# Performance work log

Measured on AMD Instinct MI355X. Metric: run time of the kernel, lower is better.

The kernel has to match this reference:

```python
import jax, jax.numpy as jnp
import numpy as np

NUM_GROUPS = 32
EPS = 1e-6

def group_norm(x, gamma, beta):
    # x: [B, C, P]
    B, C, P = x.shape
    xg = x.reshape(B, NUM_GROUPS, C // NUM_GROUPS, P)
    mean = jnp.mean(xg, axis=(2, 3), keepdims=True)
    var = jnp.var(xg, axis=(2, 3), keepdims=True)
    xn = ((xg - mean) * jax.lax.rsqrt(var + EPS)).reshape(B, C, P)
    return xn * gamma[None, :, None] + beta[None, :, None]

def conv1x1(h, w, b):
    # h: [B, C, P], w: [C_out, C_in], b: [C_out]
    return jnp.einsum('oc,bcp->bop', w, h) + b[None, :, None]

def setup_inputs() -> dict:
    key = jax.random.key(0)
    ks = jax.random.split(key, 10)
    B, C, P = 4, 512, 4096
    x = jax.random.normal(ks[0], (B, C, P), dtype=jnp.float32)
    gn_gamma = jnp.ones((C,), dtype=jnp.float32)
    gn_beta = jnp.zeros((C,), dtype=jnp.float32)
    s = 0.02
    wq = jax.random.normal(ks[1], (C, C), dtype=jnp.float32) * s
    bq = jax.random.normal(ks[2], (C,), dtype=jnp.float32) * s
    wk = jax.random.normal(ks[3], (C, C), dtype=jnp.float32) * s
    bk = jax.random.normal(ks[4], (C,), dtype=jnp.float32) * s
    wv = jax.random.normal(ks[5], (C, C), dtype=jnp.float32) * s
    bv = jax.random.normal(ks[6], (C,), dtype=jnp.float32) * s
    wo = jax.random.normal(ks[7], (C, C), dtype=jnp.float32) * s
    bo = jax.random.normal(ks[8], (C,), dtype=jnp.float32) * s
    return {"x": x, "gn_gamma": gn_gamma, "gn_beta": gn_beta,
            "wq": wq, "bq": bq, "wk": wk, "bk": bk,
            "wv": wv, "bv": bv, "wo": wo, "bo": bo}

def reference(x, gn_gamma, gn_beta, wq, bq, wk, bk, wv, bv, wo, bo):
    h = group_norm(x, gn_gamma, gn_beta)          # [B, C, P]
    q = conv1x1(h, wq, bq)                         # [B, C, P]
    k = conv1x1(h, wk, bk)                         # [B, C, P]
    v = conv1x1(h, wv, bv)                         # [B, C, P]
    C = q.shape[1]
    scale = 1.0 / jnp.sqrt(jnp.float32(C))
    # w[b, i, j] = sum_c q[b, c, i] * k[b, c, j]
    w = jnp.einsum('bci,bcj->bij', q, k) * scale   # [B, P, P]
    w = jax.nn.softmax(w, axis=2)
    # h_out[b, c, i] = sum_j v[b, c, j] * w[b, i, j]
    h = jnp.einsum('bij,bcj->bci', w, v)           # [B, C, P]
    h = conv1x1(h, wo, bo)
    return x + h
```

## Files before the change

### kernel.cpp

```cpp
#include <hip/hip_runtime.h>
#include <stdint.h>


typedef __bf16 bf16_t;
typedef __attribute__((ext_vector_type(4))) __bf16 bf16x4;
typedef __attribute__((ext_vector_type(8))) __bf16 bf16x8;
typedef __attribute__((ext_vector_type(4))) float floatx4;
typedef __attribute__((ext_vector_type(8))) int intx8;

constexpr int CDIM = 512;
constexpr int PDIM = 4096;

__device__ __forceinline__ void ld_g2l(const void* g, void* l) {
  __builtin_amdgcn_global_load_lds(
      (const __attribute__((address_space(1))) void*)g,
      (__attribute__((address_space(3))) void*)l,
      16, 0, 0);
}

__device__ __forceinline__ uint32_t pk_fp8x4(float a, float b, float c,
                                             float d) {
  int r = __builtin_amdgcn_cvt_pk_fp8_f32(a, b, 0, false);
  r = __builtin_amdgcn_cvt_pk_fp8_f32(c, d, r, true);
  return (uint32_t)r;
}

__device__ __forceinline__ int sigma_row(int r) {
  return (r & 64) + ((r & 15) << 2) + ((r >> 4) & 3);
}

enum { EPI_QK = 0, EPI_V = 1, EPI_OUT = 4, EPI_EXP = 2, EPI_PV = 5 };

template <int EPI, int TM>
__global__ __launch_bounds__(256) void gemm_tn(
    const bf16_t* __restrict__ A, const bf16_t* __restrict__ B, int K,
    int lda, int ldb, long sAb, long sBb, long sCb, void* __restrict__ Cv,
    int ldc, const float* __restrict__ bias, const float* __restrict__ xres) {
  constexpr int MI = TM / 32;
  constexpr int WROWS = TM / 2;
  __shared__ bf16_t Asm[TM * 64];
  __shared__ bf16_t Bsm[128 * 64];

  const int tid = threadIdx.x;
  const int w = tid >> 6, l = tid & 63;
  const int m0 = blockIdx.y * TM, n0 = blockIdx.x * 128;
  const int bz = blockIdx.z;

  const bf16_t* Ab = A + (long)bz * sAb + (long)m0 * lda;
  const bf16_t* Bb = B + (long)bz * sBb + (long)n0 * ldb;

  const int r0 = 8 * w + (l >> 3);
  const int schunk = (l & 7) ^ (l >> 3);
  const bf16_t* ga = Ab + (long)r0 * lda + schunk * 8;
  bf16_t* lA = Asm + (8 * w) * 64;
  bf16_t* lB = Bsm + (8 * w) * 64;

  const int wr = w >> 1, wc = w & 1;
  const int fr = l & 15, fq = l >> 4, l7 = l & 7;

  floatx4 acc[MI][4];
  floatx4 zz = {0.f, 0.f, 0.f, 0.f};
#pragma unroll
  for (int i = 0; i < MI; i++)
#pragma unroll
    for (int j = 0; j < 4; j++) acc[i][j] = zz;

  for (int kb = 0; kb < K; kb += 64) {
#pragma unroll
    for (int p = 0; p < 4; p++) {
      if (p < TM / 32) ld_g2l(ga + (long)p * 32 * lda + kb, lA + p * 2048);
      const int sig = sigma_row(r0 + 32 * p);
      ld_g2l(Bb + (long)sig * ldb + schunk * 8 + kb, lB + p * 2048);
    }
    __syncthreads();
#pragma unroll
    for (int ks = 0; ks < 2; ks++) {
      bf16x8 af[MI], bfv[4];
      const int ch = (ks * 4 + fq);
#pragma unroll
      for (int mi = 0; mi < MI; mi++) {
        int row = wr * WROWS + mi * 16 + fr;
        af[mi] = *(const bf16x8*)(Asm + row * 64 + ((ch ^ l7) * 8));
      }
#pragma unroll
      for (int ni = 0; ni < 4; ni++) {
        int row = wc * 64 + ni * 16 + fr;
        bfv[ni] = *(const bf16x8*)(Bsm + row * 64 + ((ch ^ l7) * 8));
      }
#pragma unroll
      for (int mi = 0; mi < MI; mi++)
#pragma unroll
        for (int ni = 0; ni < 4; ni++)
          acc[mi][ni] = __builtin_amdgcn_mfma_f32_16x16x32_bf16(
              af[mi], bfv[ni], acc[mi][ni], 0, 0, 0);
    }
    __syncthreads();
  }

  const int rb = fq * 4;
  const int gcolb = n0 + wc * 64 + 4 * fr;
#pragma unroll
  for (int mi = 0; mi < MI; mi++) {
#pragma unroll
    for (int i = 0; i < 4; i++) {
      const int grow = m0 + wr * WROWS + mi * 16 + rb + i;
      float v0 = acc[mi][0][i], v1 = acc[mi][1][i];
      float v2 = acc[mi][2][i], v3 = acc[mi][3][i];
      if constexpr (EPI == EPI_QK) {
        const float4 b4 = *(const float4*)(bias + gcolb);
        *(uint32_t*)((uint8_t*)Cv + (long)bz * sCb + (long)grow * ldc +
                     gcolb) =
            pk_fp8x4(v0 + b4.x, v1 + b4.y, v2 + b4.z, v3 + b4.w);
      } else if constexpr (EPI == EPI_V) {
        const float bb = bias[grow];
        uint32_t d = pk_fp8x4(v0 + bb, v1 + bb, v2 + bb, v3 + bb);
        *(uint32_t*)((uint8_t*)Cv + (long)bz * sCb + (long)grow * ldc +
                     gcolb) = d;
      } else {
        int ob = gcolb >> 12, op = gcolb & 4095;
        long o = ((long)ob * CDIM + grow) * PDIM + op;
        const float4 xr = *(const float4*)(xres + o);
        const float bb = bias[grow];
        float4 ov = {v0 + bb + xr.x, v1 + bb + xr.y, v2 + bb + xr.z,
                     v3 + bb + xr.w};
        *(float4*)((float*)Cv + o) = ov;
      }
    }
  }
}

template <int EPI, int TM, int SA>
__global__ __launch_bounds__(256) void gemm_f8(
    const uint8_t* __restrict__ A, const uint8_t* __restrict__ B, int K,
    int lda, int ldb, long sAb, long sBb, long sCb, void* __restrict__ Cv,
    int ldc, float* __restrict__ rsum) {
  constexpr int MI = TM / 32;
  constexpr int WROWS = TM / 2;
  __shared__ uint8_t Asm[TM * 128];
  __shared__ uint8_t Bsm[128 * 128];

  const int tid = threadIdx.x;
  const int w = tid >> 6, l = tid & 63;
  const int m0 = blockIdx.y * TM, n0 = blockIdx.x * 128;
  const int bz = blockIdx.z;

  const uint8_t* Ab = A + (long)bz * sAb + (long)m0 * lda;
  const uint8_t* Bb = B + (long)bz * sBb + (long)n0 * ldb;

  const int r0 = 8 * w + (l >> 3);
  const int schunk = (l & 7) ^ (l >> 3);
  const uint8_t* ga = Ab + (long)r0 * lda + schunk * 16;
  uint8_t* lA = Asm + (8 * w) * 128;
  uint8_t* lB = Bsm + (8 * w) * 128;

  const int wr = w >> 1, wc = w & 1;
  const int fr = l & 15, fq = l >> 4, l7 = l & 7;

  floatx4 acc[MI][4];
#pragma unroll
  for (int i = 0; i < MI; i++)
#pragma unroll
    for (int j = 0; j < 4; j++) acc[i][j] = floatx4{0.f, 0.f, 0.f, 0.f};

  const int s0 = ((2 * fq) ^ l7) * 16;
  const int s1 = ((2 * fq + 1) ^ l7) * 16;

  for (int kb = 0; kb < K; kb += 128) {
#pragma unroll
    for (int p = 0; p < 4; p++) {
      if (p < MI) ld_g2l(ga + (long)p * 32 * lda + kb, lA + p * 4096);
      const int sig = sigma_row(r0 + 32 * p);
      ld_g2l(Bb + (long)sig * ldb + schunk * 16 + kb, lB + p * 4096);
    }
    __syncthreads();

    intx8 af[MI];
#pragma unroll
    for (int mi = 0; mi < MI; mi++) {
      const uint8_t* base = Asm + (wr * WROWS + mi * 16 + fr) * 128;
      uint4 x0 = *(const uint4*)(base + s0);
      uint4 x1 = *(const uint4*)(base + s1);
      af[mi] = intx8{(int)x0.x, (int)x0.y, (int)x0.z, (int)x0.w,
                     (int)x1.x, (int)x1.y, (int)x1.z, (int)x1.w};
    }
#pragma unroll
    for (int ni = 0; ni < 4; ni++) {
      const uint8_t* base = Bsm + (wc * 64 + ni * 16 + fr) * 128;
      uint4 y0 = *(const uint4*)(base + s0);
      uint4 y1 = *(const uint4*)(base + s1);
      intx8 bf = intx8{(int)y0.x, (int)y0.y, (int)y0.z, (int)y0.w,
                       (int)y1.x, (int)y1.y, (int)y1.z, (int)y1.w};
#pragma unroll
      for (int mi = 0; mi < MI; mi++)
        acc[mi][ni] = __builtin_amdgcn_mfma_scale_f32_16x16x128_f8f6f4(
            af[mi], bf, acc[mi][ni], 0, 0, 0, SA, 0, 127);
    }
    __syncthreads();
  }

  const int rb = fq * 4;
  const int gcolb = n0 + wc * 64 + 4 * fr;
#pragma unroll
  for (int mi = 0; mi < MI; mi++) {
#pragma unroll
    for (int i = 0; i < 4; i++) {
      const int grow = m0 + wr * WROWS + mi * 16 + rb + i;
      if constexpr (EPI == EPI_EXP) {
        float p0 = exp2f(acc[mi][0][i]), p1 = exp2f(acc[mi][1][i]);
        float p2 = exp2f(acc[mi][2][i]), p3 = exp2f(acc[mi][3][i]);
        *(uint32_t*)((uint8_t*)Cv + (long)bz * sCb + (long)grow * ldc +
                     gcolb) = pk_fp8x4(p0, p1, p2, p3);
        float rowacc = (p0 + p1) + (p2 + p3);
        rowacc += __shfl_xor(rowacc, 1);
        rowacc += __shfl_xor(rowacc, 2);
        rowacc += __shfl_xor(rowacc, 4);
        rowacc += __shfl_xor(rowacc, 8);
        if (fr == 0) atomicAdd(&rsum[(long)bz * PDIM + grow], rowacc);
      } else {
        const float inv =
            __builtin_amdgcn_rcpf(rsum[(long)bz * PDIM + grow]);
        bf16x4 o = {(bf16_t)(acc[mi][0][i] * inv),
                    (bf16_t)(acc[mi][1][i] * inv),
                    (bf16_t)(acc[mi][2][i] * inv),
                    (bf16_t)(acc[mi][3][i] * inv)};
        *(bf16x4*)((bf16_t*)Cv + (long)bz * sCb + (long)grow * ldc + gcolb) =
            o;
      }
    }
  }
}

__global__ __launch_bounds__(256) void gn_stats(const float* __restrict__ x,
                                                float2* __restrict__ part) {
  const int i = blockIdx.x;
  const float4* xp = (const float4*)(x + (long)i * 8192);
  float s0 = 0.f, s1 = 0.f;
  for (int j = threadIdx.x; j < 2048; j += 256) {
    float4 v = xp[j];
    s0 += v.x + v.y + v.z + v.w;
    s1 += v.x * v.x + v.y * v.y + v.z * v.z + v.w * v.w;
  }
  for (int o = 32; o; o >>= 1) {
    s0 += __shfl_xor(s0, o);
    s1 += __shfl_xor(s1, o);
  }
  __shared__ float r0[4], r1[4];
  if ((threadIdx.x & 63) == 0) {
    r0[threadIdx.x >> 6] = s0;
    r1[threadIdx.x >> 6] = s1;
  }
  __syncthreads();
  if (threadIdx.x == 0)
    part[i] = make_float2(r0[0] + r0[1] + r0[2] + r0[3],
                          r1[0] + r1[1] + r1[2] + r1[3]);
}

__global__ __launch_bounds__(256) void gn_norm(
    const float* __restrict__ x, const float* __restrict__ gamma,
    const float* __restrict__ beta, const float2* __restrict__ part,
    bf16_t* __restrict__ h_t) {
  const int b = blockIdx.x >> 7;
  const int p0 = (blockIdx.x & 127) * 32;
  const int t = threadIdx.x;
  __shared__ float gmS[512], btS[512];
  __shared__ float gmean[32], grstd[32];
  __shared__ __align__(16) bf16_t tile[32 * 520];

  if (t < 32) {
    const float2* pp = part + (b * 32 + t) * 8;
    float s0 = 0.f, s1 = 0.f;
#pragma unroll
    for (int s = 0; s < 8; s++) {
      float2 v = pp[s];
      s0 += v.x;
      s1 += v.y;
    }
    float mean = s0 * (1.f / 65536.f);
    float var = s1 * (1.f / 65536.f) - mean * mean;
    gmean[t] = mean;
    grstd[t] = rsqrtf(var + 1e-6f);
  }
  __syncthreads();
  for (int c = t; c < 512; c += 256) {
    float g = gamma[c] * grstd[c >> 4];
    gmS[c] = g;
    btS[c] = beta[c] - gmean[c >> 4] * g;
  }
  __syncthreads();

  const int cc = t >> 3, pcol = (t & 7) * 4;
  for (int pass = 0; pass < 16; pass++) {
    int c = pass * 32 + cc;
    float4 v = *(const float4*)(x + ((long)(b * 512 + c)) * 4096 + p0 + pcol);
    float g = gmS[c], bb = btS[c];
    tile[(pcol + 0) * 520 + c] = (bf16_t)(v.x * g + bb);
    tile[(pcol + 1) * 520 + c] = (bf16_t)(v.y * g + bb);
    tile[(pcol + 2) * 520 + c] = (bf16_t)(v.z * g + bb);
    tile[(pcol + 3) * 520 + c] = (bf16_t)(v.w * g + bb);
  }
  __syncthreads();
  const int p = t >> 3;
  bf16_t* orow = h_t + ((long)(b * 4096 + p0 + p)) * 512;
  const bf16_t* trow = tile + p * 520;
#pragma unroll
  for (int j = 0; j < 8; j++) {
    int ch = (t & 7) + 8 * j;
    *(uint4*)(orow + ch * 8) = *(const uint4*)(trow + ch * 8);
  }
}

__global__ __launch_bounds__(256) void cvt_weights(
    const float* __restrict__ wq, const float* __restrict__ wk,
    const float* __restrict__ wv, const float* __restrict__ wo,
    const float* __restrict__ bq, const float* __restrict__ bk,
    bf16_t* __restrict__ out, float* __restrict__ bqk) {
  constexpr float QW = 1.02013936f;
  int i = blockIdx.x * 256 + threadIdx.x;
  out[i] = (bf16_t)(wq[i] * QW);
  out[262144 + i] = (bf16_t)wk[i];
  out[2 * 262144 + i] = (bf16_t)wv[i];
  out[3 * 262144 + i] = (bf16_t)wo[i];
  if (i < 512)
    bqk[i] = bq[i] * QW;
  else if (i < 1024)
    bqk[i] = bk[i - 512];
}

extern "C" void kernel_launch(void* const* d_in, const int* in_sizes, int n_in,
                              void* d_out, int out_size, void* d_ws,
                              size_t ws_size, hipStream_t stream) {
  const float* x = (const float*)d_in[0];
  const float* gamma = (const float*)d_in[1];
  const float* beta = (const float*)d_in[2];
  const float* wq = (const float*)d_in[3];
  const float* bq = (const float*)d_in[4];
  const float* wk = (const float*)d_in[5];
  const float* bk = (const float*)d_in[6];
  const float* wv = (const float*)d_in[7];
  const float* bv = (const float*)d_in[8];
  const float* wo = (const float*)d_in[9];
  const float* bo = (const float*)d_in[10];

  char* ws = (char*)d_ws;
  bf16_t* h_t = (bf16_t*)(ws);
  uint8_t* qk8 = (uint8_t*)(ws + (16l << 20));
  uint8_t* v_c = (uint8_t*)(ws + (48l << 20));
  bf16_t* h_at = (bf16_t*)(ws + (64l << 20));
  bf16_t* w_b = (bf16_t*)(ws + (80l << 20));
  float2* part = (float2*)(ws + (83l << 20));
  float* bqk = (float*)(ws + (83l << 20) + (64l << 10));
  float* rsum = (float*)(ws + (83l << 20) + (128l << 10));
  uint8_t* Sbuf = (uint8_t*)(ws + (84l << 20));

  const long sQK8 = (long)PDIM * 1024;
  const long sS = (long)PDIM * PDIM;

  hipMemsetAsync(rsum, 0, 4 * PDIM * sizeof(float), stream);
  cvt_weights<<<1024, 256, 0, stream>>>(wq, wk, wv, wo, bq, bk, w_b, bqk);
  gn_stats<<<1024, 256, 0, stream>>>(x, part);
  gn_norm<<<512, 256, 0, stream>>>(x, gamma, beta, part, h_t);
  gemm_tn<EPI_QK, 128><<<dim3(8, 128, 1), 256, 0, stream>>>(
      h_t, w_b, 512, 512, 512, 0, 0, 0, qk8, 1024, bqk, nullptr);
  gemm_tn<EPI_V, 64><<<dim3(128, 8, 1), 256, 0, stream>>>(
      w_b + 2 * 262144, h_t, 512, 512, 512, 0, 0, 0, v_c, 16384, bv, nullptr);
  gemm_f8<EPI_EXP, 128, 123><<<dim3(32, 32, 4), 256, 0, stream>>>(
      qk8, qk8 + 512, 512, 1024, 1024, sQK8, sQK8, sS, Sbuf, 4096, rsum);
  gemm_f8<EPI_PV, 64, 127><<<dim3(4, 64, 4), 256, 0, stream>>>(
      Sbuf, v_c, 4096, 4096, 16384, sS, 4096, (long)PDIM * CDIM, h_at, 512,
      rsum);
  gemm_tn<EPI_OUT, 64><<<dim3(128, 8, 1), 256, 0, stream>>>(
      w_b + 3 * 262144, h_at, 512, 512, 512, 0, 0, 0, d_out, 4096, bo, x);
}
```

Before: 295.4 us.

## Enlarge GEMM tiles, add XCD-aware block remap, replace rowsum atomics with partials

The GEMM kernels are generalised to a configurable thread count, and the QK projection and QK^T exp kernels move to 256-row tiles with 512 threads. The PV kernel moves to 128-row tiles. Block indices are remapped so neighbouring tiles land on the same XCD and share L2. The atomicAdd row-sum accumulation is replaced by per-column-block partial writes plus a separate reduce kernel, which also removes the memset. The goals are less operand reloading, better L2 locality, and no atomic contention, at the cost of higher register and LDS pressure per block and one extra launch.

```diff
diff --git a/kernel.cpp b/kernel.cpp
--- a/kernel.cpp
+++ b/kernel.cpp
@@ -29,22 +29,39 @@
   return (r & 64) + ((r & 15) << 2) + ((r >> 4) & 3);
 }
 
+__device__ __forceinline__ void xcd_remap(int& bx, int& by, int& bz) {
+  const int gx = gridDim.x, gy = gridDim.y;
+  const int nwg = gx * gy * (int)gridDim.z;
+  int lin = bx + gx * (by + gy * bz);
+  int wg = (lin & 7) * (nwg >> 3) + (lin >> 3);
+  bx = wg % gx;
+  int t = wg / gx;
+  by = t % gy;
+  bz = t / gy;
+}
+
 enum { EPI_QK = 0, EPI_V = 1, EPI_OUT = 4, EPI_EXP = 2, EPI_PV = 5 };
 
-template <int EPI, int TM>
-__global__ __launch_bounds__(256) void gemm_tn(
+template <int EPI, int TM, int NT, bool SWZ>
+__global__ __launch_bounds__(NT) void gemm_tn(
     const bf16_t* __restrict__ A, const bf16_t* __restrict__ B, int K,
     int lda, int ldb, long sAb, long sBb, long sCb, void* __restrict__ Cv,
     int ldc, const float* __restrict__ bias, const float* __restrict__ xres) {
-  constexpr int MI = TM / 32;
-  constexpr int WROWS = TM / 2;
+  constexpr int NW = NT / 64;
+  constexpr int WROWS = TM / (NW / 2);
+  constexpr int MI = WROWS / 16;
+  constexpr int RB = NT / 8;
+  constexpr int AB = TM / RB;
+  constexpr int BB = 128 / RB;
+  constexpr int PMAX = AB > BB ? AB : BB;
   __shared__ bf16_t Asm[TM * 64];
   __shared__ bf16_t Bsm[128 * 64];
 
   const int tid = threadIdx.x;
   const int w = tid >> 6, l = tid & 63;
-  const int m0 = blockIdx.y * TM, n0 = blockIdx.x * 128;
-  const int bz = blockIdx.z;
+  int bx = blockIdx.x, by = blockIdx.y, bz = blockIdx.z;
+  if constexpr (SWZ) xcd_remap(bx, by, bz);
+  const int m0 = by * TM, n0 = bx * 128;
 
   const bf16_t* Ab = A + (long)bz * sAb + (long)m0 * lda;
   const bf16_t* Bb = B + (long)bz * sBb + (long)n0 * ldb;
@@ -67,10 +84,12 @@
 
   for (int kb = 0; kb < K; kb += 64) {
 #pragma unroll
-    for (int p = 0; p < 4; p++) {
-      if (p < TM / 32) ld_g2l(ga + (long)p * 32 * lda + kb, lA + p * 2048);
-      const int sig = sigma_row(r0 + 32 * p);
-      ld_g2l(Bb + (long)sig * ldb + schunk * 8 + kb, lB + p * 2048);
+    for (int p = 0; p < PMAX; p++) {
+      if (p < AB) ld_g2l(ga + (long)(p * RB) * lda + kb, lA + p * RB * 64);
+      if (p < BB) {
+        const int sig = sigma_row(r0 + RB * p);
+        ld_g2l(Bb + (long)sig * ldb + schunk * 8 + kb, lB + p * RB * 64);
+      }
     }
     __syncthreads();
 #pragma unroll
@@ -129,20 +148,26 @@
   }
 }
 
-template <int EPI, int TM, int SA>
-__global__ __launch_bounds__(256) void gemm_f8(
+template <int EPI, int TM, int SA, int NT>
+__global__ __launch_bounds__(NT) void gemm_f8(
     const uint8_t* __restrict__ A, const uint8_t* __restrict__ B, int K,
     int lda, int ldb, long sAb, long sBb, long sCb, void* __restrict__ Cv,
     int ldc, float* __restrict__ rsum) {
-  constexpr int MI = TM / 32;
-  constexpr int WROWS = TM / 2;
+  constexpr int NW = NT / 64;
+  constexpr int WROWS = TM / (NW / 2);
+  constexpr int MI = WROWS / 16;
+  constexpr int RB = NT / 8;
+  constexpr int AB = TM / RB;
+  constexpr int BB = 128 / RB;
+  constexpr int PMAX = AB > BB ? AB : BB;
   __shared__ uint8_t Asm[TM * 128];
   __shared__ uint8_t Bsm[128 * 128];
 
   const int tid = threadIdx.x;
   const int w = tid >> 6, l = tid & 63;
-  const int m0 = blockIdx.y * TM, n0 = blockIdx.x * 128;
-  const int bz = blockIdx.z;
+  int bx = blockIdx.x, by = blockIdx.y, bz = blockIdx.z;
+  xcd_remap(bx, by, bz);
+  const int m0 = by * TM, n0 = bx * 128;
 
   const uint8_t* Ab = A + (long)bz * sAb + (long)m0 * lda;
   const uint8_t* Bb = B + (long)bz * sBb + (long)n0 * ldb;
@@ -167,10 +192,12 @@
 
   for (int kb = 0; kb < K; kb += 128) {
 #pragma unroll
-    for (int p = 0; p < 4; p++) {
-      if (p < MI) ld_g2l(ga + (long)p * 32 * lda + kb, lA + p * 4096);
-      const int sig = sigma_row(r0 + 32 * p);
-      ld_g2l(Bb + (long)sig * ldb + schunk * 16 + kb, lB + p * 4096);
+    for (int p = 0; p < PMAX; p++) {
+      if (p < AB) ld_g2l(ga + (long)(p * RB) * lda + kb, lA + p * RB * 128);
+      if (p < BB) {
+        const int sig = sigma_row(r0 + RB * p);
+        ld_g2l(Bb + (long)sig * ldb + schunk * 16 + kb, lB + p * RB * 128);
+      }
     }
     __syncthreads();
 
@@ -215,7 +242,8 @@
         rowacc += __shfl_xor(rowacc, 2);
         rowacc += __shfl_xor(rowacc, 4);
         rowacc += __shfl_xor(rowacc, 8);
-        if (fr == 0) atomicAdd(&rsum[(long)bz * PDIM + grow], rowacc);
+        if (fr == 0)
+          rsum[((long)(bz * 64 + bx * 2 + wc)) * PDIM + grow] = rowacc;
       } else {
         const float inv =
             __builtin_amdgcn_rcpf(rsum[(long)bz * PDIM + grow]);
@@ -228,6 +256,17 @@
       }
     }
   }
+}
+
+__global__ __launch_bounds__(256) void rsum_reduce(
+    const float* __restrict__ part2, float* __restrict__ rsum) {
+  const int r = blockIdx.x * 256 + threadIdx.x;
+  const int bz = r >> 12, row = r & 4095;
+  const float* p = part2 + ((long)bz * 64) * PDIM + row;
+  float s = 0.f;
+#pragma unroll
+  for (int j = 0; j < 64; j++) s += p[(long)j * PDIM];
+  rsum[r] = s;
 }
 
 __global__ __launch_bounds__(256) void gn_stats(const float* __restrict__ x,
@@ -343,6 +382,7 @@
 
   char* ws = (char*)d_ws;
   bf16_t* h_t = (bf16_t*)(ws);
+  float* part2 = (float*)(ws);
   uint8_t* qk8 = (uint8_t*)(ws + (16l << 20));
   uint8_t* v_c = (uint8_t*)(ws + (48l << 20));
   bf16_t* h_at = (bf16_t*)(ws + (64l << 20));
@@ -355,19 +395,19 @@
   const long sQK8 = (long)PDIM * 1024;
   const long sS = (long)PDIM * PDIM;
 
-  hipMemsetAsync(rsum, 0, 4 * PDIM * sizeof(float), stream);
   cvt_weights<<<1024, 256, 0, stream>>>(wq, wk, wv, wo, bq, bk, w_b, bqk);
   gn_stats<<<1024, 256, 0, stream>>>(x, part);
   gn_norm<<<512, 256, 0, stream>>>(x, gamma, beta, part, h_t);
-  gemm_tn<EPI_QK, 128><<<dim3(8, 128, 1), 256, 0, stream>>>(
+  gemm_tn<EPI_QK, 256, 512, true><<<dim3(8, 64, 1), 512, 0, stream>>>(
       h_t, w_b, 512, 512, 512, 0, 0, 0, qk8, 1024, bqk, nullptr);
-  gemm_tn<EPI_V, 64><<<dim3(128, 8, 1), 256, 0, stream>>>(
+  gemm_tn<EPI_V, 64, 256, false><<<dim3(128, 8, 1), 256, 0, stream>>>(
       w_b + 2 * 262144, h_t, 512, 512, 512, 0, 0, 0, v_c, 16384, bv, nullptr);
-  gemm_f8<EPI_EXP, 128, 123><<<dim3(32, 32, 4), 256, 0, stream>>>(
-      qk8, qk8 + 512, 512, 1024, 1024, sQK8, sQK8, sS, Sbuf, 4096, rsum);
-  gemm_f8<EPI_PV, 64, 127><<<dim3(4, 64, 4), 256, 0, stream>>>(
+  gemm_f8<EPI_EXP, 256, 123, 512><<<dim3(32, 16, 4), 512, 0, stream>>>(
+      qk8, qk8 + 512, 512, 1024, 1024, sQK8, sQK8, sS, Sbuf, 4096, part2);
+  rsum_reduce<<<64, 256, 0, stream>>>(part2, rsum);
+  gemm_f8<EPI_PV, 128, 127, 256><<<dim3(4, 32, 4), 256, 0, stream>>>(
       Sbuf, v_c, 4096, 4096, 16384, sS, 4096, (long)PDIM * CDIM, h_at, 512,
       rsum);
-  gemm_tn<EPI_OUT, 64><<<dim3(128, 8, 1), 256, 0, stream>>>(
+  gemm_tn<EPI_OUT, 64, 256, false><<<dim3(128, 8, 1), 256, 0, stream>>>(
       w_b + 3 * 262144, h_at, 512, 512, 512, 0, 0, 0, d_out, 4096, bo, x);
 }
```

New measurement: 304.8 us. 3.2% more time.
